# Kernel optimization log

Measured on AMD Instinct MI355X. Metric: run time of the kernel, lower is better.

## Reference

```python
import jax, jax.numpy as jnp
import numpy as np

NEG = jnp.float32(-1e30)  # finite stand-in for -inf in masked max
SLOPE = 0.01              # F.leaky_relu default negative slope


def _lrelu(v):
    return jnp.where(v >= 0, v, SLOPE * v)


def _mlp(pts, w1, b1, w2, b2, w3, b3):
    # pts: [2, N] -> [64, N]; 1x1 Conv1d == pointwise linear over channel dim
    z = _lrelu(w1 @ pts + b1[:, None])
    z = _lrelu(w2 @ z + b2[:, None])
    z = _lrelu(w3 @ z + b3[:, None])
    return z


def setup_inputs() -> dict:
    key = jax.random.key(0)
    ks = jax.random.split(key, 10)
    B, C, H, W = 4, 19, 256, 256
    x = jax.random.randint(ks[0], (B, C, H, W), 0, 2, dtype=jnp.int32)
    # grid exactly as in the torch module: meshgrid of two linspaces, flattened
    g = np.array(np.meshgrid(np.linspace(-1, 1, 256), np.linspace(-1, 1, 256),
                             sparse=False)).astype(np.float32)  # [2,256,256]
    grid = jnp.asarray(g.reshape(2, -1))  # [2, 65536]
    w1 = jax.random.normal(ks[1], (64, 2), jnp.float32) * 0.5
    b1 = jax.random.normal(ks[2], (64,), jnp.float32) * 0.1
    w2 = jax.random.normal(ks[3], (64, 64), jnp.float32) * 0.125
    b2 = jax.random.normal(ks[4], (64,), jnp.float32) * 0.1
    w3 = jax.random.normal(ks[5], (64, 64), jnp.float32) * 0.125
    b3 = jax.random.normal(ks[6], (64,), jnp.float32) * 0.1
    fcw = jax.random.normal(ks[7], (512, 64 * C), jnp.float32)
    fcb = jax.random.normal(ks[8], (512,), jnp.float32) * 0.1
    return {"x": x, "grid": grid, "w1": w1, "b1": b1, "w2": w2, "b2": b2,
            "w3": w3, "b3": b3, "fcw": fcw, "fcb": fcb}


def reference(x, grid, w1, b1, w2, b2, w3, b3, fcw, fcb):
    B, C = x.shape[0], x.shape[1]
    # Pointwise MLP on the shared grid once (grid identical for all b,c)
    feats = _mlp(grid, w1, b1, w2, b2, w3, b3)                 # [64, N]
    # Fallback feature for empty masks: MLP on a single zero point
    zero_feat = _mlp(jnp.zeros((2, 1), feats.dtype),
                     w1, b1, w2, b2, w3, b3)[:, 0]             # [64]
    mask = (x.reshape(B, C, -1) == 1)                          # [B, C, N]
    # Masked max over the ragged point sets, fully vectorized
    masked = jnp.where(mask[:, :, None, :], feats[None, None], NEG)
    z = jnp.max(masked, axis=-1)                               # [B, C, 64]
    empty = ~jnp.any(mask, axis=-1)                            # [B, C]
    z = jnp.where(empty[..., None], zero_feat, z)
    flat = z.reshape(B, C * 64)                                # channel-major cat
    # EqualLinear: weight scaled by 1/sqrt(in_dim) (lr_mul=1)
    scale = jnp.float32(1.0 / np.sqrt(C * 64))
    out = flat @ (fcw * scale).T + fcb                         # [B, 512]
    return jnp.repeat(out[:, None, :], 18, axis=1)             # [B, 18, 512]
```

## Files before the change

### kernel.cpp

```cpp
#include <hip/hip_runtime.h>

#define NPTS  65536
#define NBC   76
#define NEGF  (-1e30f)

__device__ __forceinline__ float lrelu(float v) { return v >= 0.0f ? v : 0.01f * v; }

__device__ __forceinline__ unsigned fkey(float f) {
  unsigned u = __float_as_uint(f);
  return (u & 0x80000000u) ? ~u : (u | 0x80000000u);
}
__device__ __forceinline__ float fdec(unsigned k) {
  return (k & 0x80000000u) ? __uint_as_float(k & 0x7fffffffu) : __uint_as_float(~k);
}

#define MLP_LAYER(WT, BS)                                                     \
  {                                                                           \
    float s[4][4];                                                            \
    _Pragma("unroll")                                                         \
    for (int a = 0; a < 4; ++a)                                               \
      _Pragma("unroll")                                                       \
      for (int b = 0; b < 4; ++b) s[a][b] = 0.0f;                             \
    _Pragma("unroll 4")                                                       \
    for (int k = 0; k < 64; ++k) {                                            \
      float4 av = *reinterpret_cast<const float4*>(&WT[k * 64 + j0]);         \
      float4 bv = *reinterpret_cast<const float4*>(&zt[k * 68 + p0]);         \
      float aa[4] = {av.x, av.y, av.z, av.w};                                 \
      float bb[4] = {bv.x, bv.y, bv.z, bv.w};                                 \
      _Pragma("unroll")                                                       \
      for (int a = 0; a < 4; ++a)                                             \
        _Pragma("unroll")                                                     \
        for (int b = 0; b < 4; ++b) s[a][b] += aa[a] * bb[b];                 \
    }                                                                         \
    __syncthreads();                                                          \
    _Pragma("unroll")                                                         \
    for (int jj = 0; jj < 4; ++jj) {                                          \
      float bias = BS[j0 + jj];                                               \
      float4 z;                                                               \
      z.x = lrelu(s[jj][0] + bias);                                           \
      z.y = lrelu(s[jj][1] + bias);                                           \
      z.z = lrelu(s[jj][2] + bias);                                           \
      z.w = lrelu(s[jj][3] + bias);                                           \
      *reinterpret_cast<float4*>(&zt[(j0 + jj) * 68 + p0]) = z;               \
    }                                                                         \
    __syncthreads();                                                          \
  }

__global__ __launch_bounds__(256) void k1_fused(
    const int* __restrict__ x, const float* __restrict__ grid,
    const float* __restrict__ w1, const float* __restrict__ b1,
    const float* __restrict__ w2, const float* __restrict__ b2,
    const float* __restrict__ w3, const float* __restrict__ b3,
    unsigned* __restrict__ keys, float* __restrict__ zfeat)
{
  __shared__ __align__(16) float w1s[128];
  __shared__ float b1s[64], b2s[64], b3s[64];
  __shared__ __align__(16) float w2t[4096];
  __shared__ __align__(16) float w3t[4096];
  __shared__ __align__(16) float zt[64 * 68];
  __shared__ unsigned long long mbits[NBC];
  __shared__ float zf1[64], zf2[64];

  const int t = threadIdx.x;

  if (t < 128) w1s[t] = w1[t];
  if (t < 64) { b1s[t] = b1[t]; b2s[t] = b2[t]; b3s[t] = b3[t]; }
  for (int idx = t; idx < 4096; idx += 256) {
    int k = idx >> 6, j = idx & 63;
    w2t[idx] = w2[j * 64 + k];
    w3t[idx] = w3[j * 64 + k];
  }
  __syncthreads();

  if (blockIdx.x == 0) {
    if (t < 64) zf1[t] = lrelu(b1s[t]);
    __syncthreads();
    if (t < 64) {
      float a = b2s[t];
      for (int k = 0; k < 64; ++k) a += w2t[k * 64 + t] * zf1[k];
      zf2[t] = lrelu(a);
    }
    __syncthreads();
    if (t < 64) {
      float a = b3s[t];
      for (int k = 0; k < 64; ++k) a += w3t[k * 64 + t] * zf2[k];
      zfeat[t] = lrelu(a);
    }
  }

  const int tk = t >> 4, tp = t & 15;
  const int j0 = tk * 4, p0 = tp * 4;
  const int kq = t & 15, bg = t >> 4;
  const int bcbase = bg * 5;

  float acc[5][4];
  #pragma unroll
  for (int ii = 0; ii < 5; ++ii)
    #pragma unroll
    for (int i = 0; i < 4; ++i) acc[ii][i] = NEGF;

  for (int tile = 0; tile < 2; ++tile) {
    const int n0 = blockIdx.x * 128 + tile * 64;

    float4 g0 = *reinterpret_cast<const float4*>(grid + n0 + p0);
    float4 g1 = *reinterpret_cast<const float4*>(grid + NPTS + n0 + p0);
    #pragma unroll
    for (int kk = 0; kk < 4; ++kk) {
      int k = j0 + kk;
      float a0 = w1s[2 * k], a1 = w1s[2 * k + 1], bb = b1s[k];
      float4 z;
      z.x = lrelu(a0 * g0.x + a1 * g1.x + bb);
      z.y = lrelu(a0 * g0.y + a1 * g1.y + bb);
      z.z = lrelu(a0 * g0.z + a1 * g1.z + bb);
      z.w = lrelu(a0 * g0.w + a1 * g1.w + bb);
      *reinterpret_cast<float4*>(&zt[k * 68 + p0]) = z;
    }
    __syncthreads();

    MLP_LAYER(w2t, b2s)
    MLP_LAYER(w3t, b3s)

    {
      const int wv = t >> 6, lane = t & 63;
      for (int bc = wv; bc < NBC; bc += 4) {
        int v = x[(bc << 16) + n0 + lane];
        unsigned long long m = __ballot(v == 1);
        if (lane == 0) mbits[bc] = m;
      }
    }
    __syncthreads();

    {
      unsigned mlo[5], mhi[5];
      #pragma unroll
      for (int ii = 0; ii < 5; ++ii) {
        int bc = bcbase + ii;
        unsigned long long m = (bc < NBC) ? mbits[bc] : 0ull;
        mlo[ii] = (unsigned)m;
        mhi[ii] = (unsigned)(m >> 32);
      }
      #pragma unroll 4
      for (int n = 0; n < 32; ++n) {
        float f0 = zt[(kq)      * 68 + n];
        float f1 = zt[(kq + 16) * 68 + n];
        float f2 = zt[(kq + 32) * 68 + n];
        float f3 = zt[(kq + 48) * 68 + n];
        float h0 = zt[(kq)      * 68 + n + 32];
        float h1 = zt[(kq + 16) * 68 + n + 32];
        float h2 = zt[(kq + 32) * 68 + n + 32];
        float h3 = zt[(kq + 48) * 68 + n + 32];
        #pragma unroll
        for (int ii = 0; ii < 5; ++ii) {
          bool bl = (mlo[ii] >> n) & 1u;
          acc[ii][0] = fmaxf(acc[ii][0], bl ? f0 : NEGF);
          acc[ii][1] = fmaxf(acc[ii][1], bl ? f1 : NEGF);
          acc[ii][2] = fmaxf(acc[ii][2], bl ? f2 : NEGF);
          acc[ii][3] = fmaxf(acc[ii][3], bl ? f3 : NEGF);
          bool bh = (mhi[ii] >> n) & 1u;
          acc[ii][0] = fmaxf(acc[ii][0], bh ? h0 : NEGF);
          acc[ii][1] = fmaxf(acc[ii][1], bh ? h1 : NEGF);
          acc[ii][2] = fmaxf(acc[ii][2], bh ? h2 : NEGF);
          acc[ii][3] = fmaxf(acc[ii][3], bh ? h3 : NEGF);
        }
      }
    }
    __syncthreads();
  }

  #pragma unroll
  for (int ii = 0; ii < 5; ++ii) {
    int bc = bcbase + ii;
    if (bc < NBC) {
      #pragma unroll
      for (int i = 0; i < 4; ++i) {
        float v = acc[ii][i];
        if (v > -5e29f) atomicMax(&keys[bc * 64 + kq + 16 * i], fkey(v));
      }
    }
  }
}

__global__ __launch_bounds__(256) void k2_fc(
    const unsigned* __restrict__ keys, const float* __restrict__ zfeat,
    const float* __restrict__ fcw, const float* __restrict__ fcb,
    float* __restrict__ out)
{
  __shared__ float flat[4864];
  const int t = threadIdx.x;
  for (int idx = t; idx < 4864; idx += 256) {
    unsigned k = keys[idx];
    flat[idx] = (k == 0u) ? zfeat[idx & 63] : fdec(k);
  }
  __syncthreads();

  const int wv = t >> 6, lane = t & 63;
  const int o = blockIdx.x * 4 + wv;
  const float* wrow = fcw + o * 1216;
  float fa0 = 0.f, fa1 = 0.f, fa2 = 0.f, fa3 = 0.f;
  #pragma unroll
  for (int i = 0; i < 19; ++i) {
    int jj = i * 64 + lane;
    float wvv = wrow[jj];
    fa0 += wvv * flat[jj];
    fa1 += wvv * flat[1216 + jj];
    fa2 += wvv * flat[2432 + jj];
    fa3 += wvv * flat[3648 + jj];
  }
  #pragma unroll
  for (int off = 32; off > 0; off >>= 1) {
    fa0 += __shfl_xor(fa0, off);
    fa1 += __shfl_xor(fa1, off);
    fa2 += __shfl_xor(fa2, off);
    fa3 += __shfl_xor(fa3, off);
  }
  const float scale = 0.028676966733820225f;
  float cb = fcb[o];
  if (lane < 18) {
    out[(0 * 18 + lane) * 512 + o] = fa0 * scale + cb;
    out[(1 * 18 + lane) * 512 + o] = fa1 * scale + cb;
    out[(2 * 18 + lane) * 512 + o] = fa2 * scale + cb;
    out[(3 * 18 + lane) * 512 + o] = fa3 * scale + cb;
  }
}

extern "C" void kernel_launch(void* const* d_in, const int* in_sizes, int n_in,
                              void* d_out, int out_size, void* d_ws, size_t ws_size,
                              hipStream_t stream)
{
  const int*   x    = (const int*)d_in[0];
  const float* grid = (const float*)d_in[1];
  const float* w1   = (const float*)d_in[2];
  const float* b1   = (const float*)d_in[3];
  const float* w2   = (const float*)d_in[4];
  const float* b2   = (const float*)d_in[5];
  const float* w3   = (const float*)d_in[6];
  const float* b3   = (const float*)d_in[7];
  const float* fcw  = (const float*)d_in[8];
  const float* fcb  = (const float*)d_in[9];
  float* out = (float*)d_out;

  unsigned* keys = (unsigned*)d_ws;
  float* zfeat   = (float*)d_ws + 4864;

  hipMemsetAsync(d_ws, 0, 4864 * sizeof(unsigned), stream);
  hipLaunchKernelGGL(k1_fused, dim3(512), dim3(256), 0, stream,
                     x, grid, w1, b1, w2, b2, w3, b3, keys, zfeat);
  hipLaunchKernelGGL(k2_fc, dim3(128), dim3(256), 0, stream,
                     keys, zfeat, fcw, fcb, out);
}
```

Measured before the change: 148.6 us.

## Restructure fused MLP/masked-max kernel with scalar weights, integer max and replicated atomics

Result: faster. 145.7 us (-2.0%).

```diff
diff --git a/kernel.cpp b/kernel.cpp
--- a/kernel.cpp
+++ b/kernel.cpp
@@ -2,7 +2,8 @@
 
 #define NPTS  65536
 #define NBC   76
-#define NEGF  (-1e30f)
+#define NREP  8
+#define KEYN  4864
 
 __device__ __forceinline__ float lrelu(float v) { return v >= 0.0f ? v : 0.01f * v; }
 
@@ -13,183 +14,174 @@
 __device__ __forceinline__ float fdec(unsigned k) {
   return (k & 0x80000000u) ? __uint_as_float(k & 0x7fffffffu) : __uint_as_float(~k);
 }
-
-#define MLP_LAYER(WT, BS)                                                     \
-  {                                                                           \
-    float s[4][4];                                                            \
-    _Pragma("unroll")                                                         \
-    for (int a = 0; a < 4; ++a)                                               \
-      _Pragma("unroll")                                                       \
-      for (int b = 0; b < 4; ++b) s[a][b] = 0.0f;                             \
-    _Pragma("unroll 4")                                                       \
-    for (int k = 0; k < 64; ++k) {                                            \
-      float4 av = *reinterpret_cast<const float4*>(&WT[k * 64 + j0]);         \
-      float4 bv = *reinterpret_cast<const float4*>(&zt[k * 68 + p0]);         \
-      float aa[4] = {av.x, av.y, av.z, av.w};                                 \
-      float bb[4] = {bv.x, bv.y, bv.z, bv.w};                                 \
-      _Pragma("unroll")                                                       \
-      for (int a = 0; a < 4; ++a)                                             \
-        _Pragma("unroll")                                                     \
-        for (int b = 0; b < 4; ++b) s[a][b] += aa[a] * bb[b];                 \
-    }                                                                         \
-    __syncthreads();                                                          \
-    _Pragma("unroll")                                                         \
-    for (int jj = 0; jj < 4; ++jj) {                                          \
-      float bias = BS[j0 + jj];                                               \
-      float4 z;                                                               \
-      z.x = lrelu(s[jj][0] + bias);                                           \
-      z.y = lrelu(s[jj][1] + bias);                                           \
-      z.z = lrelu(s[jj][2] + bias);                                           \
-      z.w = lrelu(s[jj][3] + bias);                                           \
-      *reinterpret_cast<float4*>(&zt[(j0 + jj) * 68 + p0]) = z;               \
-    }                                                                         \
-    __syncthreads();                                                          \
-  }
 
 __global__ __launch_bounds__(256) void k1_fused(
     const int* __restrict__ x, const float* __restrict__ grid,
     const float* __restrict__ w1, const float* __restrict__ b1,
     const float* __restrict__ w2, const float* __restrict__ b2,
     const float* __restrict__ w3, const float* __restrict__ b3,
-    unsigned* __restrict__ keys, float* __restrict__ zfeat)
+    unsigned* __restrict__ keys)
 {
-  __shared__ __align__(16) float w1s[128];
-  __shared__ float b1s[64], b2s[64], b3s[64];
-  __shared__ __align__(16) float w2t[4096];
-  __shared__ __align__(16) float w3t[4096];
-  __shared__ __align__(16) float zt[64 * 68];
+  __shared__ unsigned zt[64 * 68];
   __shared__ unsigned long long mbits[NBC];
-  __shared__ float zf1[64], zf2[64];
-
-  const int t = threadIdx.x;
-
-  if (t < 128) w1s[t] = w1[t];
-  if (t < 64) { b1s[t] = b1[t]; b2s[t] = b2[t]; b3s[t] = b3[t]; }
-  for (int idx = t; idx < 4096; idx += 256) {
-    int k = idx >> 6, j = idx & 63;
-    w2t[idx] = w2[j * 64 + k];
-    w3t[idx] = w3[j * 64 + k];
-  }
-  __syncthreads();
-
-  if (blockIdx.x == 0) {
-    if (t < 64) zf1[t] = lrelu(b1s[t]);
-    __syncthreads();
-    if (t < 64) {
-      float a = b2s[t];
-      for (int k = 0; k < 64; ++k) a += w2t[k * 64 + t] * zf1[k];
-      zf2[t] = lrelu(a);
-    }
-    __syncthreads();
-    if (t < 64) {
-      float a = b3s[t];
-      for (int k = 0; k < 64; ++k) a += w3t[k * 64 + t] * zf2[k];
-      zfeat[t] = lrelu(a);
-    }
-  }
-
-  const int tk = t >> 4, tp = t & 15;
-  const int j0 = tk * 4, p0 = tp * 4;
+
+  const int t    = threadIdx.x;
+  const int lane = t & 63;
+  const int wv   = t >> 6;
+  const int n0   = blockIdx.x * 64;
+
+  {
+    int bc0 = wv * 19;
+    #pragma unroll
+    for (int i = 0; i < 19; ++i) {
+      int bc = bc0 + i;
+      int v = x[(bc << 16) + n0 + lane];
+      unsigned long long m = __ballot(v == 1);
+      if (lane == 0) mbits[bc] = m;
+    }
+  }
+
+  const int jb = __builtin_amdgcn_readfirstlane(wv * 16);
+
+  {
+    float g0 = grid[n0 + lane];
+    float g1 = grid[NPTS + n0 + lane];
+    #pragma unroll
+    for (int jj = 0; jj < 16; ++jj) {
+      int j = jb + jj;
+      float z = lrelu(w1[2 * j] * g0 + w1[2 * j + 1] * g1 + b1[j]);
+      zt[j * 68 + lane] = __float_as_uint(z);
+    }
+  }
+  __syncthreads();
+
+  float acc[16];
+
+  #pragma unroll
+  for (int jj = 0; jj < 16; ++jj) acc[jj] = b2[jb + jj];
+  #pragma unroll 4
+  for (int k = 0; k < 64; ++k) {
+    float zv = __uint_as_float(zt[k * 68 + lane]);
+    #pragma unroll
+    for (int jj = 0; jj < 16; ++jj) acc[jj] += w2[(jb + jj) * 64 + k] * zv;
+  }
+  __syncthreads();
+  #pragma unroll
+  for (int jj = 0; jj < 16; ++jj)
+    zt[(jb + jj) * 68 + lane] = __float_as_uint(lrelu(acc[jj]));
+  __syncthreads();
+
+  #pragma unroll
+  for (int jj = 0; jj < 16; ++jj) acc[jj] = b3[jb + jj];
+  #pragma unroll 4
+  for (int k = 0; k < 64; ++k) {
+    float zv = __uint_as_float(zt[k * 68 + lane]);
+    #pragma unroll
+    for (int jj = 0; jj < 16; ++jj) acc[jj] += w3[(jb + jj) * 64 + k] * zv;
+  }
+  __syncthreads();
+  #pragma unroll
+  for (int jj = 0; jj < 16; ++jj)
+    zt[(jb + jj) * 68 + lane] = fkey(lrelu(acc[jj]));
+  __syncthreads();
+
   const int kq = t & 15, bg = t >> 4;
   const int bcbase = bg * 5;
 
-  float acc[5][4];
+  unsigned mlo[5], mhi[5];
+  #pragma unroll
+  for (int ii = 0; ii < 5; ++ii) {
+    int bc = bcbase + ii;
+    unsigned long long m = (bc < NBC) ? mbits[bc] : 0ull;
+    mlo[ii] = (unsigned)m;
+    mhi[ii] = (unsigned)(m >> 32);
+  }
+
+  unsigned uacc[5][4];
   #pragma unroll
   for (int ii = 0; ii < 5; ++ii)
     #pragma unroll
-    for (int i = 0; i < 4; ++i) acc[ii][i] = NEGF;
-
-  for (int tile = 0; tile < 2; ++tile) {
-    const int n0 = blockIdx.x * 128 + tile * 64;
-
-    float4 g0 = *reinterpret_cast<const float4*>(grid + n0 + p0);
-    float4 g1 = *reinterpret_cast<const float4*>(grid + NPTS + n0 + p0);
-    #pragma unroll
-    for (int kk = 0; kk < 4; ++kk) {
-      int k = j0 + kk;
-      float a0 = w1s[2 * k], a1 = w1s[2 * k + 1], bb = b1s[k];
-      float4 z;
-      z.x = lrelu(a0 * g0.x + a1 * g1.x + bb);
-      z.y = lrelu(a0 * g0.y + a1 * g1.y + bb);
-      z.z = lrelu(a0 * g0.z + a1 * g1.z + bb);
-      z.w = lrelu(a0 * g0.w + a1 * g1.w + bb);
-      *reinterpret_cast<float4*>(&zt[k * 68 + p0]) = z;
-    }
-    __syncthreads();
-
-    MLP_LAYER(w2t, b2s)
-    MLP_LAYER(w3t, b3s)
-
-    {
-      const int wv = t >> 6, lane = t & 63;
-      for (int bc = wv; bc < NBC; bc += 4) {
-        int v = x[(bc << 16) + n0 + lane];
-        unsigned long long m = __ballot(v == 1);
-        if (lane == 0) mbits[bc] = m;
+    for (int i = 0; i < 4; ++i) uacc[ii][i] = 0u;
+
+  #pragma unroll 2
+  for (int np = 0; np < 8; ++np) {
+    const int n = np * 4;
+    uint4 lo[4], hi[4];
+    #pragma unroll
+    for (int i = 0; i < 4; ++i) {
+      lo[i] = *reinterpret_cast<const uint4*>(&zt[(kq + 16 * i) * 68 + n]);
+      hi[i] = *reinterpret_cast<const uint4*>(&zt[(kq + 16 * i) * 68 + n + 32]);
+    }
+    #pragma unroll
+    for (int ii = 0; ii < 5; ++ii) {
+      unsigned sl0 = (unsigned)((int)(mlo[ii] << (31 - n)) >> 31);
+      unsigned sl1 = (unsigned)((int)(mlo[ii] << (30 - n)) >> 31);
+      unsigned sl2 = (unsigned)((int)(mlo[ii] << (29 - n)) >> 31);
+      unsigned sl3 = (unsigned)((int)(mlo[ii] << (28 - n)) >> 31);
+      unsigned sh0 = (unsigned)((int)(mhi[ii] << (31 - n)) >> 31);
+      unsigned sh1 = (unsigned)((int)(mhi[ii] << (30 - n)) >> 31);
+      unsigned sh2 = (unsigned)((int)(mhi[ii] << (29 - n)) >> 31);
+      unsigned sh3 = (unsigned)((int)(mhi[ii] << (28 - n)) >> 31);
+      #pragma unroll
+      for (int i = 0; i < 4; ++i) {
+        unsigned a = uacc[ii][i];
+        a = max(max(a, lo[i].x & sl0), lo[i].y & sl1);
+        a = max(max(a, lo[i].z & sl2), lo[i].w & sl3);
+        a = max(max(a, hi[i].x & sh0), hi[i].y & sh1);
+        a = max(max(a, hi[i].z & sh2), hi[i].w & sh3);
+        uacc[ii][i] = a;
       }
     }
-    __syncthreads();
-
-    {
-      unsigned mlo[5], mhi[5];
-      #pragma unroll
-      for (int ii = 0; ii < 5; ++ii) {
-        int bc = bcbase + ii;
-        unsigned long long m = (bc < NBC) ? mbits[bc] : 0ull;
-        mlo[ii] = (unsigned)m;
-        mhi[ii] = (unsigned)(m >> 32);
-      }
-      #pragma unroll 4
-      for (int n = 0; n < 32; ++n) {
-        float f0 = zt[(kq)      * 68 + n];
-        float f1 = zt[(kq + 16) * 68 + n];
-        float f2 = zt[(kq + 32) * 68 + n];
-        float f3 = zt[(kq + 48) * 68 + n];
-        float h0 = zt[(kq)      * 68 + n + 32];
-        float h1 = zt[(kq + 16) * 68 + n + 32];
-        float h2 = zt[(kq + 32) * 68 + n + 32];
-        float h3 = zt[(kq + 48) * 68 + n + 32];
-        #pragma unroll
-        for (int ii = 0; ii < 5; ++ii) {
-          bool bl = (mlo[ii] >> n) & 1u;
-          acc[ii][0] = fmaxf(acc[ii][0], bl ? f0 : NEGF);
-          acc[ii][1] = fmaxf(acc[ii][1], bl ? f1 : NEGF);
-          acc[ii][2] = fmaxf(acc[ii][2], bl ? f2 : NEGF);
-          acc[ii][3] = fmaxf(acc[ii][3], bl ? f3 : NEGF);
-          bool bh = (mhi[ii] >> n) & 1u;
-          acc[ii][0] = fmaxf(acc[ii][0], bh ? h0 : NEGF);
-          acc[ii][1] = fmaxf(acc[ii][1], bh ? h1 : NEGF);
-          acc[ii][2] = fmaxf(acc[ii][2], bh ? h2 : NEGF);
-          acc[ii][3] = fmaxf(acc[ii][3], bh ? h3 : NEGF);
-        }
-      }
-    }
-    __syncthreads();
-  }
-
+  }
+
+  unsigned* krep = keys + (blockIdx.x & (NREP - 1)) * KEYN;
   #pragma unroll
   for (int ii = 0; ii < 5; ++ii) {
     int bc = bcbase + ii;
     if (bc < NBC) {
       #pragma unroll
       for (int i = 0; i < 4; ++i) {
-        float v = acc[ii][i];
-        if (v > -5e29f) atomicMax(&keys[bc * 64 + kq + 16 * i], fkey(v));
+        unsigned v = uacc[ii][i];
+        if (v) atomicMax(&krep[bc * 64 + kq + 16 * i], v);
       }
     }
   }
 }
 
 __global__ __launch_bounds__(256) void k2_fc(
-    const unsigned* __restrict__ keys, const float* __restrict__ zfeat,
+    const unsigned* __restrict__ keys,
+    const float* __restrict__ b1, const float* __restrict__ w2,
+    const float* __restrict__ b2, const float* __restrict__ w3,
+    const float* __restrict__ b3,
     const float* __restrict__ fcw, const float* __restrict__ fcb,
     float* __restrict__ out)
 {
   __shared__ float flat[4864];
+  __shared__ float za[64], zb[64], zf[64];
   const int t = threadIdx.x;
+
+  if (t < 64) za[t] = lrelu(b1[t]);
+  __syncthreads();
+  if (t < 64) {
+    float s = b2[t];
+    #pragma unroll 8
+    for (int k = 0; k < 64; ++k) s += w2[t * 64 + k] * za[k];
+    zb[t] = lrelu(s);
+  }
+  __syncthreads();
+  if (t < 64) {
+    float s = b3[t];
+    #pragma unroll 8
+    for (int k = 0; k < 64; ++k) s += w3[t * 64 + k] * zb[k];
+    zf[t] = lrelu(s);
+  }
+  __syncthreads();
+
   for (int idx = t; idx < 4864; idx += 256) {
-    unsigned k = keys[idx];
-    flat[idx] = (k == 0u) ? zfeat[idx & 63] : fdec(k);
+    unsigned m = keys[idx];
+    #pragma unroll
+    for (int r = 1; r < NREP; ++r) m = max(m, keys[r * KEYN + idx]);
+    flat[idx] = m ? fdec(m) : zf[idx & 63];
   }
   __syncthreads();
 
@@ -240,11 +232,10 @@
   float* out = (float*)d_out;
 
   unsigned* keys = (unsigned*)d_ws;
-  float* zfeat   = (float*)d_ws + 4864;
-
-  hipMemsetAsync(d_ws, 0, 4864 * sizeof(unsigned), stream);
-  hipLaunchKernelGGL(k1_fused, dim3(512), dim3(256), 0, stream,
-                     x, grid, w1, b1, w2, b2, w3, b3, keys, zfeat);
+
+  hipMemsetAsync(d_ws, 0, NREP * KEYN * sizeof(unsigned), stream);
+  hipLaunchKernelGGL(k1_fused, dim3(1024), dim3(256), 0, stream,
+                     x, grid, w1, b1, w2, b2, w3, b3, keys);
   hipLaunchKernelGGL(k2_fc, dim3(128), dim3(256), 0, stream,
-                     keys, zfeat, fcw, fcb, out);
-}
+                     keys, b1, w2, b2, w3, b3, fcw, fcb, out);
+}
```
